# Kernel optimization log

Hardware: AMD Instinct MI355X
Metric: run time of the kernel (lower is better)

The kernel has to match this reference:

```python
import jax, jax.numpy as jnp
import numpy as np

LN_EPS = 1e-12


def layer_norm(x, g, b):
    mu = jnp.mean(x, axis=-1, keepdims=True)
    var = jnp.mean(jnp.square(x - mu), axis=-1, keepdims=True)
    return (x - mu) * jax.lax.rsqrt(var + LN_EPS) * g + b


def setup_inputs() -> dict:
    key = jax.random.key(0)
    ks = jax.random.split(key, 12)
    B, L, H, P, V = 8, 512, 768, 200, 30522
    src_scores = jax.random.normal(ks[0], (B, L, L), jnp.float32)
    seq_hidden = jax.random.normal(ks[1], (B, L, H), jnp.float32)
    seq_mask = jax.random.randint(ks[2], (B, L), 0, 2).astype(jnp.float32)
    pos_emb = jax.random.normal(ks[3], (512, P), jnp.float32) * 0.02
    Wp = jax.random.normal(ks[4], (H, P), jnp.float32) * 0.02
    bp = jnp.zeros((H,), jnp.float32)
    Wt = jax.random.normal(ks[5], (H, H), jnp.float32) * 0.02
    bt = jnp.zeros((H,), jnp.float32)
    ln_g = jnp.ones((H,), jnp.float32)
    ln_b = jnp.zeros((H,), jnp.float32)
    Wd = jax.random.normal(ks[6], (V, H), jnp.float32) * 0.02
    dec_bias = jnp.zeros((V,), jnp.float32)
    return dict(src_scores=src_scores, seq_hidden=seq_hidden, seq_mask=seq_mask,
                pos_emb=pos_emb, Wp=Wp, bp=bp, Wt=Wt, bt=bt,
                ln_g=ln_g, ln_b=ln_b, Wd=Wd, dec_bias=dec_bias)


def reference(src_scores, seq_hidden, seq_mask, pos_emb, Wp, bp, Wt, bt, ln_g, ln_b, Wd, dec_bias):
    L = src_scores.shape[1]
    # position embeddings for first L positions, projected to hidden size: [L, H]
    pos_h = pos_emb[:L] @ Wp.T + bp
    # pos_scores[b, l, s] = pos_h[l] . seq_hidden[b, s]
    pos_scores = jnp.einsum('lh,bsh->bls', pos_h, seq_hidden)
    scores = pos_scores + src_scores + seq_mask[:, None, :] * -10000.0
    alpha = jax.nn.softmax(scores, axis=-1)                 # [B, L, L]
    seq_sum = jnp.einsum('bls,bsh->blh', alpha, seq_hidden)  # [B, L, H]
    # BertPredictionHeadTransform: dense -> gelu (exact) -> LayerNorm
    h = layer_norm(jax.nn.gelu(seq_sum @ Wt.T + bt, approximate=False), ln_g, ln_b)
    target_scores = h @ Wd.T + dec_bias                      # [B, L, V]
    return target_scores
```

## Files before the change

### kernel.cpp

```cpp
#include <hip/hip_runtime.h>

using f32x4  = __attribute__((ext_vector_type(4))) float;
using short8 = __attribute__((ext_vector_type(8))) short;
using short4v= __attribute__((ext_vector_type(4))) short;
typedef __attribute__((ext_vector_type(8))) __bf16 bf16x8;

__device__ static inline short f2bf(float f){
    unsigned u = __builtin_bit_cast(unsigned, f);
    u += 0x7fffu + ((u >> 16) & 1u);
    return (short)(u >> 16);
}

__device__ static inline void gload_lds16(const void* g, void* l){
    __builtin_amdgcn_global_load_lds(
        (const __attribute__((address_space(1))) void*)g,
        (__attribute__((address_space(3))) void*)l, 16, 0, 0);
}

#define BKK 64

template<int EPI, bool SWZ, bool MFAST>
__global__ __launch_bounds__(256, 2)
void gemm_bt(const short* __restrict__ A, const short* __restrict__ B,
             float* __restrict__ outF, short* __restrict__ outB,
             const float* __restrict__ bias,
             const float* __restrict__ addmat, const float* __restrict__ mask,
             int K, int ldc, int Ncheck,
             long sA, long sB, long sC, long sX, int maskStride)
{
    __shared__ short Abuf[128*BKK];
    __shared__ short Bbuf[128*BKK];
    const int tid  = threadIdx.x;
    const int wave = tid >> 6;
    const int lane = tid & 63;
    const int bz   = blockIdx.z;

    int bx = blockIdx.x, by = blockIdx.y;
    if constexpr (SWZ) {
        const unsigned GX   = gridDim.x;
        const unsigned nwg  = GX * gridDim.y;
        const unsigned orig = blockIdx.y * GX + blockIdx.x;
        const unsigned q = nwg >> 3, r = nwg & 7;
        const unsigned xcd = orig & 7, pos = orig >> 3;
        const unsigned w = (xcd < r ? xcd*(q+1) : r*(q+1) + (xcd-r)*q) + pos;
        bx = w % GX; by = w / GX;
    }
    const int m0 = (MFAST ? bx : by) * 128;
    const int n0 = (MFAST ? by : bx) * 128;
    const short* Ab = A + (long)bz * sA;
    const short* Bb = B + (long)bz * sB;

    const int wr = (wave >> 1) * 64;
    const int wc = (wave &  1) * 64;

    f32x4 acc[4][4];
    #pragma unroll
    for (int i=0;i<4;++i)
        #pragma unroll
        for (int j=0;j<4;++j) acc[i][j] = (f32x4){0.f,0.f,0.f,0.f};

    const int srow = wave*32 + (lane >> 3);
    const int kch  = (lane & 7) ^ (lane >> 3);
    const short* gA = Ab + (long)(m0 + srow)*K + kch*8;
    const short* gB = Bb + (long)(n0 + srow)*K + kch*8;
    short* lA = Abuf + wave*32*BKK;
    short* lB = Bbuf + wave*32*BKK;

    for (int k0 = 0; k0 < K; k0 += BKK) {
        __syncthreads();
        #pragma unroll
        for (int is=0; is<4; ++is){
            gload_lds16(gA + k0 + (long)is*8*K, lA + is*8*BKK);
            gload_lds16(gB + k0 + (long)is*8*K, lB + is*8*BKK);
        }
        __syncthreads();
        #pragma unroll
        for (int ks=0; ks<2; ++ks){
            bf16x8 af[4], bfr[4];
            const int chunk = ks*4 + (lane >> 4);
            #pragma unroll
            for (int mi=0;mi<4;++mi){
                int row = wr + mi*16 + (lane & 15);
                af[mi] = *(const bf16x8*)((const char*)Abuf + row*128 + ((chunk ^ (row & 7))<<4));
            }
            #pragma unroll
            for (int ni=0;ni<4;++ni){
                int row = wc + ni*16 + (lane & 15);
                bfr[ni] = *(const bf16x8*)((const char*)Bbuf + row*128 + ((chunk ^ (row & 7))<<4));
            }
            #pragma unroll
            for (int mi=0;mi<4;++mi)
                #pragma unroll
                for (int ni=0;ni<4;++ni)
                    acc[mi][ni] = __builtin_amdgcn_mfma_f32_16x16x32_bf16(af[mi], bfr[ni], acc[mi][ni], 0, 0, 0);
        }
    }

    const int rb = (lane >> 4) * 4;
    const int cb = lane & 15;
    #pragma unroll
    for (int mi=0;mi<4;++mi){
        #pragma unroll
        for (int r=0;r<4;++r){
            const int row = m0 + wr + mi*16 + rb + r;
            #pragma unroll
            for (int ni=0;ni<4;++ni){
                const int col = n0 + wc + ni*16 + cb;
                float v = acc[mi][ni][r];
                if constexpr (EPI == 0) {
                    v += addmat[(long)bz*sX + (long)row*ldc + col]
                         - 10000.f * mask[bz*maskStride + col];
                    outF[(long)bz*sC + (long)row*ldc + col] = v;
                } else if constexpr (EPI == 1) {
                    outB[(long)bz*sC + (long)row*ldc + col] = f2bf(v);
                } else if constexpr (EPI == 3) {
                    if (col < Ncheck) outF[(long)row*ldc + col] = v + bias[col];
                } else if constexpr (EPI == 4) {
                    outB[(long)row*ldc + col] = f2bf(v + bias[col]);
                }
            }
        }
    }
}

__global__ __launch_bounds__(256)
void conv_bf16(const float* __restrict__ in, short* __restrict__ out, long n, long ntot)
{
    const long stride = (long)gridDim.x * 2048;
    for (long i = ((long)blockIdx.x*256 + threadIdx.x)*8; i < ntot; i += stride){
        short8 o = (short8){0,0,0,0,0,0,0,0};
        if (i < n){
            f32x4 a = *(const f32x4*)(in + i);
            f32x4 b = *(const f32x4*)(in + i + 4);
            o[0]=f2bf(a[0]); o[1]=f2bf(a[1]); o[2]=f2bf(a[2]); o[3]=f2bf(a[3]);
            o[4]=f2bf(b[0]); o[5]=f2bf(b[1]); o[6]=f2bf(b[2]); o[7]=f2bf(b[3]);
        }
        *(short8*)(out + i) = o;
    }
}

__global__ __launch_bounds__(256)
void conv_pad(const float* __restrict__ in, short* __restrict__ out,
              int Cin, int Cpad, int total)
{
    int idx = blockIdx.x*256 + threadIdx.x;
    if (idx >= total) return;
    int r = idx / Cpad, c = idx - r*Cpad;
    short v = 0;
    if (c < Cin) v = f2bf(in[(long)r*Cin + c]);
    out[idx] = v;
}

__global__ __launch_bounds__(256)
void transpose_to_bf16(const float* __restrict__ in, short* __restrict__ out, int R, int C)
{
    __shared__ float t[32][33];
    const long boff = (long)blockIdx.z * R * C;
    const float* inb = in + boff;
    short* outb = out + boff;
    int c0 = blockIdx.x*32, r0 = blockIdx.y*32;
    int tx = threadIdx.x & 31, ty = threadIdx.x >> 5;
    #pragma unroll
    for (int j=0;j<32;j+=8) t[ty+j][tx] = inb[(long)(r0+ty+j)*C + c0+tx];
    __syncthreads();
    #pragma unroll
    for (int j=0;j<32;j+=8) outb[(long)(c0+ty+j)*R + r0+tx] = f2bf(t[tx][ty+j]);
}

__global__ __launch_bounds__(256)
void softmax_bf16(const float* __restrict__ scores, short* __restrict__ alpha, int L)
{
    const int row  = blockIdx.x*4 + (threadIdx.x >> 6);
    const int lane = threadIdx.x & 63;
    const float* p = scores + (long)row*L + lane*8;
    f32x4 v0 = *(const f32x4*)p;
    f32x4 v1 = *(const f32x4*)(p+4);
    float x[8] = {v0[0],v0[1],v0[2],v0[3],v1[0],v1[1],v1[2],v1[3]};
    float m = x[0];
    #pragma unroll
    for (int j=1;j<8;++j) m = fmaxf(m, x[j]);
    #pragma unroll
    for (int off=32; off; off>>=1) m = fmaxf(m, __shfl_xor(m, off));
    float s = 0.f;
    #pragma unroll
    for (int j=0;j<8;++j){ x[j] = __expf(x[j]-m); s += x[j]; }
    #pragma unroll
    for (int off=32; off; off>>=1) s += __shfl_xor(s, off);
    const float rinv = 1.f / s;
    short8 o;
    #pragma unroll
    for (int j=0;j<8;++j) o[j] = f2bf(x[j]*rinv);
    *(short8*)(alpha + (long)row*L + lane*8) = o;
}

__global__ __launch_bounds__(256)
void gelu_ln(const float* __restrict__ lin, short* __restrict__ h,
             const float* __restrict__ g, const float* __restrict__ b, int H)
{
    const int row  = blockIdx.x*4 + (threadIdx.x >> 6);
    const int lane = threadIdx.x & 63;
    const float* p = lin + (long)row*H;
    float x[12];
    #pragma unroll
    for (int c=0;c<3;++c){
        f32x4 v = *(const f32x4*)(p + c*256 + lane*4);
        x[c*4+0]=v[0]; x[c*4+1]=v[1]; x[c*4+2]=v[2]; x[c*4+3]=v[3];
    }
    float sum=0.f, sq=0.f;
    #pragma unroll
    for (int j=0;j<12;++j){
        float t = 0.5f * x[j] * (1.f + erff(x[j]*0.70710678118654752f));
        x[j] = t; sum += t; sq += t*t;
    }
    #pragma unroll
    for (int off=32; off; off>>=1){ sum += __shfl_xor(sum, off); sq += __shfl_xor(sq, off); }
    const float mu  = sum * (1.f/768.f);
    const float var = sq  * (1.f/768.f) - mu*mu;
    const float inv = rsqrtf(var + 1e-12f);
    #pragma unroll
    for (int c=0;c<3;++c){
        short4v o;
        #pragma unroll
        for (int j=0;j<4;++j){
            int col = c*256 + lane*4 + j;
            o[j] = f2bf((x[c*4+j]-mu)*inv*g[col] + b[col]);
        }
        *(short4v*)(h + (long)row*H + c*256 + lane*4) = o;
    }
}

extern "C" void kernel_launch(void* const* d_in, const int* in_sizes, int n_in,
                              void* d_out, int out_size, void* d_ws, size_t ws_size,
                              hipStream_t stream)
{
    const float* src_scores = (const float*)d_in[0];
    const float* seq_hidden = (const float*)d_in[1];
    const float* seq_mask   = (const float*)d_in[2];
    const float* pos_emb    = (const float*)d_in[3];
    const float* Wp         = (const float*)d_in[4];
    const float* bp         = (const float*)d_in[5];
    const float* Wt         = (const float*)d_in[6];
    const float* bt         = (const float*)d_in[7];
    const float* ln_g       = (const float*)d_in[8];
    const float* ln_b       = (const float*)d_in[9];
    const float* Wd         = (const float*)d_in[10];
    const float* dec_bias   = (const float*)d_in[11];
    float* out = (float*)d_out;

    const int B=8, L=512, H=768, V=30522, Vp=30592, Kp=256;

    const size_t need = ((size_t)Vp*H + (size_t)B*L*H) * sizeof(short);
    if (ws_size < need) return;
    short* wd_bf = (short*)d_ws;
    short* h_bf  = wd_bf + (long)Vp*H;

    char* sc = (char*)d_out;
    short* sh_nat = (short*)sc;  sc += (long)B*L*H*2;
    short* sh_t   = (short*)sc;  sc += (long)B*L*H*2;
    short* pe_p   = (short*)sc;  sc += (long)L*Kp*2;
    short* wp_p   = (short*)sc;  sc += (long)H*Kp*2;
    short* pos_h  = (short*)sc;  sc += (long)L*H*2;
    short* wt_bf  = (short*)sc;  sc += (long)H*H*2;
    float* scoresb= (float*)sc;  sc += (long)B*L*L*4;
    short* alpha  = (short*)sc;  sc += (long)B*L*L*2;
    short* seqsum = (short*)sc;  sc += (long)B*L*H*2;
    float* lin5   = (float*)sc;  sc += (long)B*L*H*4;

    {   long n=(long)V*H, ntot=(long)Vp*H;
        int blocks=(int)((ntot+2047)/2048); if (blocks>2048) blocks=2048;
        conv_bf16<<<dim3(blocks),256,0,stream>>>(Wd, wd_bf, n, ntot); }
    {   long n=(long)H*H; int blocks=(int)((n+2047)/2048);
        conv_bf16<<<dim3(blocks),256,0,stream>>>(Wt, wt_bf, n, n); }
    {   long n=(long)B*L*H; int blocks=(int)((n+2047)/2048); if (blocks>2048) blocks=2048;
        conv_bf16<<<dim3(blocks),256,0,stream>>>(seq_hidden, sh_nat, n, n); }
    transpose_to_bf16<<<dim3(H/32, L/32, B),256,0,stream>>>(seq_hidden, sh_t, L, H);
    {   int total=L*Kp;
        conv_pad<<<dim3((total+255)/256),256,0,stream>>>(pos_emb, pe_p, 200, Kp, total); }
    {   int total=H*Kp;
        conv_pad<<<dim3((total+255)/256),256,0,stream>>>(Wp, wp_p, 200, Kp, total); }

    gemm_bt<4,false,false><<<dim3(H/128, L/128, 1),256,0,stream>>>(
        pe_p, wp_p, nullptr, pos_h, bp, nullptr, nullptr,
        Kp, H, H, 0L, 0L, 0L, 0L, 0);

    gemm_bt<0,false,false><<<dim3(L/128, L/128, B),256,0,stream>>>(
        pos_h, sh_nat, scoresb, nullptr, nullptr, src_scores, seq_mask,
        H, L, L, 0L, (long)L*H, (long)L*L, (long)L*L, L);

    softmax_bf16<<<dim3(B*L/4),256,0,stream>>>(scoresb, alpha, L);

    gemm_bt<1,false,false><<<dim3(H/128, L/128, B),256,0,stream>>>(
        alpha, sh_t, nullptr, seqsum, nullptr, nullptr, nullptr,
        L, H, H, (long)L*L, (long)H*L, (long)L*H, 0L, 0);

    gemm_bt<3,false,false><<<dim3(H/128, (B*L)/128, 1),256,0,stream>>>(
        seqsum, wt_bf, lin5, nullptr, bt, nullptr, nullptr,
        H, H, H, 0L, 0L, 0L, 0L, 0);

    gelu_ln<<<dim3(B*L/4),256,0,stream>>>(lin5, h_bf, ln_g, ln_b, H);

    gemm_bt<3,true,true><<<dim3((B*L)/128, Vp/128, 1),256,0,stream>>>(
        h_bf, wd_bf, out, nullptr, dec_bias, nullptr, nullptr,
        H, V, V, 0L, 0L, 0L, 0L, 0);
}
```

Before: 504.0 us.

## Double-buffer LDS tiles in bf16 GEMM and drop XCD swizzle on decoder GEMM

The GEMM main loop now keeps two LDS buffers per operand and issues the direct global-to-LDS loads for the next K tile before computing on the current one, waiting with a partial vmcnt so the copy overlaps the MFMA work. LDS use doubles to 64 KB per block, which may limit how many blocks fit per CU under launch_bounds(256,2). Separately, the decoder GEMM grid is switched from M-fast with XCD swizzle to a plain N-fast layout, changing tile order and L2 reuse of the large weight matrix.

```diff
diff --git a/kernel.cpp b/kernel.cpp
--- a/kernel.cpp
+++ b/kernel.cpp
@@ -28,8 +28,8 @@
              int K, int ldc, int Ncheck,
              long sA, long sB, long sC, long sX, int maskStride)
 {
-    __shared__ short Abuf[128*BKK];
-    __shared__ short Bbuf[128*BKK];
+    __shared__ short Abuf[2][128*BKK];
+    __shared__ short Bbuf[2][128*BKK];
     const int tid  = threadIdx.x;
     const int wave = tid >> 6;
     const int lane = tid & 63;
@@ -63,17 +63,35 @@
     const int kch  = (lane & 7) ^ (lane >> 3);
     const short* gA = Ab + (long)(m0 + srow)*K + kch*8;
     const short* gB = Bb + (long)(n0 + srow)*K + kch*8;
-    short* lA = Abuf + wave*32*BKK;
-    short* lB = Bbuf + wave*32*BKK;
-
-    for (int k0 = 0; k0 < K; k0 += BKK) {
-        __syncthreads();
-        #pragma unroll
-        for (int is=0; is<4; ++is){
-            gload_lds16(gA + k0 + (long)is*8*K, lA + is*8*BKK);
-            gload_lds16(gB + k0 + (long)is*8*K, lB + is*8*BKK);
-        }
-        __syncthreads();
+    const int lofs = wave*32*BKK;
+
+    const int nt = K / BKK;
+
+    #pragma unroll
+    for (int is=0; is<4; ++is){
+        gload_lds16(gA + (long)is*8*K, &Abuf[0][lofs + is*8*BKK]);
+        gload_lds16(gB + (long)is*8*K, &Bbuf[0][lofs + is*8*BKK]);
+    }
+
+    for (int t = 0; t < nt; ++t) {
+        const int cur = t & 1, nxt = cur ^ 1;
+        __builtin_amdgcn_s_barrier();
+        if (t + 1 < nt) {
+            const long k1 = (long)(t + 1) * BKK;
+            #pragma unroll
+            for (int is=0; is<4; ++is){
+                gload_lds16(gA + k1 + (long)is*8*K, &Abuf[nxt][lofs + is*8*BKK]);
+                gload_lds16(gB + k1 + (long)is*8*K, &Bbuf[nxt][lofs + is*8*BKK]);
+            }
+            asm volatile("s_waitcnt vmcnt(8)" ::: "memory");
+        } else {
+            asm volatile("s_waitcnt vmcnt(0)" ::: "memory");
+        }
+        __builtin_amdgcn_s_barrier();
+        asm volatile("" ::: "memory");
+
+        const short* Ar = Abuf[cur];
+        const short* Br = Bbuf[cur];
         #pragma unroll
         for (int ks=0; ks<2; ++ks){
             bf16x8 af[4], bfr[4];
@@ -81,12 +99,12 @@
             #pragma unroll
             for (int mi=0;mi<4;++mi){
                 int row = wr + mi*16 + (lane & 15);
-                af[mi] = *(const bf16x8*)((const char*)Abuf + row*128 + ((chunk ^ (row & 7))<<4));
+                af[mi] = *(const bf16x8*)((const char*)Ar + row*128 + ((chunk ^ (row & 7))<<4));
             }
             #pragma unroll
             for (int ni=0;ni<4;++ni){
                 int row = wc + ni*16 + (lane & 15);
-                bfr[ni] = *(const bf16x8*)((const char*)Bbuf + row*128 + ((chunk ^ (row & 7))<<4));
+                bfr[ni] = *(const bf16x8*)((const char*)Br + row*128 + ((chunk ^ (row & 7))<<4));
             }
             #pragma unroll
             for (int mi=0;mi<4;++mi)
@@ -299,7 +317,7 @@
 
     gelu_ln<<<dim3(B*L/4),256,0,stream>>>(lin5, h_bf, ln_g, ln_b, H);
 
-    gemm_bt<3,true,true><<<dim3((B*L)/128, Vp/128, 1),256,0,stream>>>(
+    gemm_bt<3,false,false><<<dim3(Vp/128, (B*L)/128, 1),256,0,stream>>>(
         h_bf, wd_bf, out, nullptr, dec_bias, nullptr, nullptr,
         H, V, V, 0L, 0L, 0L, 0L, 0);
 }
```

New measurement: 550.5 us. 1.09x slower.
